# Kernel optimization log

Hardware: AMD Instinct MI355X
Metric: run time of the kernel (lower is better)

## Reference

```python
import jax, jax.numpy as jnp
import numpy as np

DIM = 768
HEADS = 12
HEAD_DIM = DIM // HEADS
B, S = 2, 2048
EPS = 1e-5


def _layernorm(x, w, b):
    mu = jnp.mean(x, axis=-1, keepdims=True)
    var = jnp.mean(jnp.square(x - mu), axis=-1, keepdims=True)
    return (x - mu) * jax.lax.rsqrt(var + EPS) * w + b


def setup_inputs() -> dict:
    key = jax.random.key(0)
    ks = jax.random.split(key, 16)
    sc = 1.0 / np.sqrt(DIM)
    inp = {
        'x': jax.random.normal(ks[0], (B, S, DIM), jnp.float32),
        'bias': jax.random.normal(ks[1], (HEADS, B, S, S), jnp.float32),
        'mask': jax.random.randint(ks[2], (1, B, S, S), 0, 2, jnp.int32),
        'ln1_w': jnp.ones((DIM,), jnp.float32),
        'ln1_b': jnp.zeros((DIM,), jnp.float32),
        'wq': jax.random.normal(ks[3], (DIM, DIM), jnp.float32) * sc,
        'bq': jnp.zeros((DIM,), jnp.float32),
        'wk': jax.random.normal(ks[4], (DIM, DIM), jnp.float32) * sc,
        'bk': jnp.zeros((DIM,), jnp.float32),
        'wv': jax.random.normal(ks[5], (DIM, DIM), jnp.float32) * sc,
        'bv': jnp.zeros((DIM,), jnp.float32),
        'wo': jax.random.normal(ks[6], (DIM, DIM), jnp.float32) * sc,
        'bo': jnp.zeros((DIM,), jnp.float32),
        'ln2_w': jnp.ones((DIM,), jnp.float32),
        'ln2_b': jnp.zeros((DIM,), jnp.float32),
        'w1': jax.random.normal(ks[7], (DIM, DIM), jnp.float32) * sc,
        'b1': jnp.zeros((DIM,), jnp.float32),
        'w2': jax.random.normal(ks[8], (DIM, DIM), jnp.float32) * sc,
        'b2': jnp.zeros((DIM,), jnp.float32),
    }
    return inp


def _split_heads(t):
    # [B,S,D] -> [H,B,S,Dh]  (matches torch view + permute(2,0,1,3))
    return t.reshape(B, S, HEADS, HEAD_DIM).transpose(2, 0, 1, 3)


def reference(x, bias, mask, ln1_w, ln1_b, wq, bq, wk, bk, wv, bv, wo, bo,
              ln2_w, ln2_b, w1, b1, w2, b2):
    xn = _layernorm(x, ln1_w, ln1_b)
    q = _split_heads(xn @ wq + bq)
    k = _split_heads(xn @ wk + bk)
    v = _split_heads(xn @ wv + bv)
    # scores: [H,B,Sq,Sk]; bias added BEFORE scaling, then masked, then scaled softmax
    scores = jnp.einsum('hbqd,hbkd->hbqk', q, k) + bias
    scores = jnp.where(mask == 0, jnp.float32(-1e20), scores)
    probs = jax.nn.softmax(scores / np.sqrt(HEAD_DIM), axis=-1)
    attn = jnp.einsum('hbqk,hbkd->hbqd', probs, v)
    attn = attn.transpose(1, 2, 0, 3).reshape(B, S, DIM)
    x = x + (attn @ wo + bo)
    xn = _layernorm(x, ln2_w, ln2_b)
    h = jax.nn.relu(xn @ w1 + b1)
    x = x + (h @ w2 + b2)
    return x
```

## Files before the change

### kernel.cpp

```cpp
#include <hip/hip_runtime.h>
#include <math.h>

#define DIMM 768
#define SEQ 2048
#define BATB 2
#define NHEAD 12
#define DHEAD 64
#define ROWS 4096

typedef __attribute__((ext_vector_type(8))) short bf16x8;
typedef __attribute__((ext_vector_type(4))) float f32x4;
typedef unsigned short ushort_t;
typedef unsigned int uint_t;

union U16 { int4 i; ushort_t u[8]; };

__device__ __forceinline__ ushort_t f2b(float f) {
    uint_t u = __float_as_uint(f);
    return (ushort_t)((u + 0x7FFFu + ((u >> 16) & 1u)) >> 16);
}

struct WPtrs { const float* s[6]; };

__global__ __launch_bounds__(256) void wtrans_k(WPtrs wp, ushort_t* __restrict__ dst)
{
    __shared__ float T[64][65];
    int wi = blockIdx.z;
    const float* in = wp.s[wi];
    ushort_t* out = dst + (size_t)wi * (DIMM * DIMM);
    int kb = blockIdx.y * 64, nb = blockIdx.x * 64;
    int t = threadIdx.x;
    int kl = t >> 4, nl = (t & 15) * 4;
    #pragma unroll
    for (int it = 0; it < 4; it++) {
        float4 a = *(const float4*)&in[(size_t)(kb + kl + it * 16) * DIMM + nb + nl];
        T[kl + it * 16][nl + 0] = a.x;
        T[kl + it * 16][nl + 1] = a.y;
        T[kl + it * 16][nl + 2] = a.z;
        T[kl + it * 16][nl + 3] = a.w;
    }
    __syncthreads();
    int no = t >> 2, ko = (t & 3) * 16;
    #pragma unroll
    for (int j = 0; j < 2; j++) {
        U16 u;
        #pragma unroll
        for (int c = 0; c < 8; c++) u.u[c] = f2b(T[ko + j * 8 + c][no]);
        *(int4*)&out[(size_t)(nb + no) * DIMM + kb + ko + j * 8] = u.i;
    }
}

__global__ __launch_bounds__(256) void ln_k(const float* __restrict__ x,
                                            const float* __restrict__ w,
                                            const float* __restrict__ b,
                                            ushort_t* __restrict__ out)
{
    int row = blockIdx.x;
    int tid = threadIdx.x;
    const float* xr = x + (size_t)row * DIMM;
    float v0 = xr[tid], v1 = xr[tid + 256], v2 = xr[tid + 512];
    float s  = v0 + v1 + v2;
    float ss = v0 * v0 + v1 * v1 + v2 * v2;
    #pragma unroll
    for (int off = 32; off > 0; off >>= 1) {
        s  += __shfl_down(s,  off);
        ss += __shfl_down(ss, off);
    }
    __shared__ float ws_[4], wss_[4];
    __shared__ float mu_s, rs_s;
    int lane = tid & 63, wid = tid >> 6;
    if (lane == 0) { ws_[wid] = s; wss_[wid] = ss; }
    __syncthreads();
    if (tid == 0) {
        float S1 = ws_[0] + ws_[1] + ws_[2] + ws_[3];
        float S2 = wss_[0] + wss_[1] + wss_[2] + wss_[3];
        float m = S1 * (1.0f / DIMM);
        float var = S2 * (1.0f / DIMM) - m * m;
        mu_s = m;
        rs_s = rsqrtf(var + 1e-5f);
    }
    __syncthreads();
    float mu = mu_s, rs = rs_s;
    ushort_t* orow = out + (size_t)row * DIMM;
    orow[tid]       = f2b((v0 - mu) * rs * w[tid]       + b[tid]);
    orow[tid + 256] = f2b((v1 - mu) * rs * w[tid + 256] + b[tid + 256]);
    orow[tid + 512] = f2b((v2 - mu) * rs * w[tid + 512] + b[tid + 512]);
}

template<int ASRC, int OMODE, bool RELU, bool RES>
__global__ __launch_bounds__(256) void mgemm_k(const ushort_t* __restrict__ A,
                                               const ushort_t* __restrict__ BT,
                                               const float* __restrict__ bias,
                                               const float* __restrict__ res,
                                               void* __restrict__ outv)
{
    __shared__ alignas(16) ushort_t Asl[8 * 64 * 8];
    __shared__ alignas(16) ushort_t Bsl[8 * 64 * 8];
    int tid = threadIdx.x;
    int lane = tid & 63, w = tid >> 6;
    int colBase = blockIdx.x * 64, rowBase = blockIdx.y * 64;

    f32x4 acc[4];
    #pragma unroll
    for (int nt = 0; nt < 4; nt++) { f32x4 z = {0.f, 0.f, 0.f, 0.f}; acc[nt] = z; }

    int sm = tid >> 2;
    int sko = (tid & 3) * 16;

    for (int kt = 0; kt < DIMM; kt += 64) {
        #pragma unroll
        for (int j = 0; j < 2; j++) {
            int k = sko + j * 8;
            size_t gidx;
            if (ASRC == 1) {
                gidx = (size_t)(rowBase + sm) * DIMM + kt + k;
            } else {
                int r = rowBase + sm, kg = kt + k;
                gidx = ((size_t)((kg >> 6) * BATB + (r >> 11)) * SEQ + (r & 2047)) * DHEAD + (kg & 63);
            }
            int4 a = *(const int4*)&A[gidx];
            int ln = (sm & 15) | (((k & 31) >> 3) << 4);
            int slot = ((sm >> 4) << 1) | (k >> 5);
            *(int4*)&Asl[(slot * 64 + ln) * 8] = a;
        }
        #pragma unroll
        for (int j = 0; j < 2; j++) {
            int k = sko + j * 8;
            int4 b = *(const int4*)&BT[(size_t)(colBase + sm) * DIMM + kt + k];
            int ln = (sm & 15) | (((k & 31) >> 3) << 4);
            int slot = (k >> 5) * 4 + (sm >> 4);
            *(int4*)&Bsl[(slot * 64 + ln) * 8] = b;
        }
        __syncthreads();
        bf16x8 a0 = *(bf16x8*)&Asl[((w * 2 + 0) * 64 + lane) * 8];
        bf16x8 a1 = *(bf16x8*)&Asl[((w * 2 + 1) * 64 + lane) * 8];
        #pragma unroll
        for (int nt = 0; nt < 4; nt++) {
            bf16x8 b0 = *(bf16x8*)&Bsl[((0 * 4 + nt) * 64 + lane) * 8];
            bf16x8 b1 = *(bf16x8*)&Bsl[((1 * 4 + nt) * 64 + lane) * 8];
            acc[nt] = __builtin_amdgcn_mfma_f32_16x16x32_bf16(a0, b0, acc[nt], 0, 0, 0);
            acc[nt] = __builtin_amdgcn_mfma_f32_16x16x32_bf16(a1, b1, acc[nt], 0, 0, 0);
        }
        __syncthreads();
    }
    int col_l = lane & 15, quad = lane >> 4;
    #pragma unroll
    for (int nt = 0; nt < 4; nt++) {
        int n = colBase + nt * 16 + col_l;
        float bn = bias[n];
        #pragma unroll
        for (int r = 0; r < 4; r++) {
            int row = rowBase + w * 16 + quad * 4 + r;
            float v = acc[nt][r] + bn;
            if (RELU) v = fmaxf(v, 0.0f);
            if (RES)  v += res[(size_t)row * DIMM + n];
            if (OMODE == 0) {
                ((float*)outv)[(size_t)row * DIMM + n] = v;
            } else if (OMODE == 1) {
                ((ushort_t*)outv)[(size_t)row * DIMM + n] = f2b(v);
            } else {
                ((ushort_t*)outv)[((size_t)((n >> 6) * BATB + (row >> 11)) * SEQ + (row & 2047)) * DHEAD + (n & 63)] = f2b(v);
            }
        }
    }
}

__global__ __launch_bounds__(256) void attn_k(const ushort_t* __restrict__ q,
                                              const ushort_t* __restrict__ k,
                                              const ushort_t* __restrict__ v,
                                              const float* __restrict__ bias,
                                              const int* __restrict__ mask,
                                              ushort_t* __restrict__ out)
{
    __shared__ alignas(16) ushort_t Kf[8 * 64 * 8];
    __shared__ alignas(16) ushort_t Vf[8 * 64 * 8];
    __shared__ alignas(16) ushort_t Pf[8 * 64 * 8];
    int tid = threadIdx.x, lane = tid & 63, w = tid >> 6;
    int col_l = lane & 15, quad = lane >> 4;
    int qbase = blockIdx.x * 64;
    int hb = blockIdx.y;
    const ushort_t* qp = q + (size_t)hb * SEQ * DHEAD;
    const ushort_t* kp = k + (size_t)hb * SEQ * DHEAD;
    const ushort_t* vp = v + (size_t)hb * SEQ * DHEAD;
    const float* bp = bias + (size_t)hb * SEQ * SEQ;
    const int*   mp = mask + (size_t)(hb & 1) * SEQ * SEQ;

    bf16x8 qF0 = *(const bf16x8*)&qp[(size_t)(qbase + w * 16 + col_l) * DHEAD + (quad * 8)];
    bf16x8 qF1 = *(const bf16x8*)&qp[(size_t)(qbase + w * 16 + col_l) * DHEAD + 32 + (quad * 8)];

    f32x4 O[4];
    #pragma unroll
    for (int nt = 0; nt < 4; nt++) { f32x4 z = {0.f, 0.f, 0.f, 0.f}; O[nt] = z; }
    float m_run[4], l_run[4];
    #pragma unroll
    for (int r = 0; r < 4; r++) { m_run[r] = -1e30f; l_run[r] = 0.0f; }

    int sn = tid >> 2, sko = (tid & 3) * 16;
    int j0 = (tid >> 3) * 2, e0 = (tid & 7) * 8;

    for (int kvb = 0; kvb < SEQ; kvb += 64) {
        #pragma unroll
        for (int jj = 0; jj < 2; jj++) {
            int kk = sko + jj * 8;
            int4 kd = *(const int4*)&kp[(size_t)(kvb + sn) * DHEAD + kk];
            int slot = (kk >> 5) * 4 + (sn >> 4);
            int ln = (sn & 15) | (((kk & 31) >> 3) << 4);
            *(int4*)&Kf[(slot * 64 + ln) * 8] = kd;
        }
        {
            U16 g0, g1;
            g0.i = *(const int4*)&vp[(size_t)(kvb + j0) * DHEAD + e0];
            g1.i = *(const int4*)&vp[(size_t)(kvb + j0 + 1) * DHEAD + e0];
            int js = j0 >> 5, grp = (j0 & 31) >> 3, i0 = j0 & 7;
            #pragma unroll
            for (int c = 0; c < 8; c++) {
                int n = e0 + c;
                uint_t pk = (uint_t)g0.u[c] | ((uint_t)g1.u[c] << 16);
                int idx = ((js * 4 + (n >> 4)) * 64 + ((n & 15) | (grp << 4))) * 8 + i0;
                *(uint_t*)&Vf[idx] = pk;
            }
        }
        float bl[4][4]; int ml[4][4];
        #pragma unroll
        for (int nt = 0; nt < 4; nt++) {
            int col = kvb + nt * 16 + col_l;
            #pragma unroll
            for (int r = 0; r < 4; r++) {
                int qrow = qbase + w * 16 + quad * 4 + r;
                bl[nt][r] = bp[(size_t)qrow * SEQ + col];
                ml[nt][r] = mp[(size_t)qrow * SEQ + col];
            }
        }
        __syncthreads();
        f32x4 S[4];
        #pragma unroll
        for (int nt = 0; nt < 4; nt++) {
            bf16x8 b0 = *(bf16x8*)&Kf[((0 * 4 + nt) * 64 + lane) * 8];
            bf16x8 b1 = *(bf16x8*)&Kf[((1 * 4 + nt) * 64 + lane) * 8];
            f32x4 z = {0.f, 0.f, 0.f, 0.f};
            z = __builtin_amdgcn_mfma_f32_16x16x32_bf16(qF0, b0, z, 0, 0, 0);
            S[nt] = __builtin_amdgcn_mfma_f32_16x16x32_bf16(qF1, b1, z, 0, 0, 0);
        }
        float lg[4][4];
        #pragma unroll
        for (int nt = 0; nt < 4; nt++)
            #pragma unroll
            for (int r = 0; r < 4; r++)
                lg[nt][r] = ml[nt][r] ? (S[nt][r] + bl[nt][r]) * 0.125f : -1.25e19f;
        float alpha[4];
        #pragma unroll
        for (int r = 0; r < 4; r++) {
            float mx = fmaxf(fmaxf(lg[0][r], lg[1][r]), fmaxf(lg[2][r], lg[3][r]));
            mx = fmaxf(mx, __shfl_xor(mx, 1));
            mx = fmaxf(mx, __shfl_xor(mx, 2));
            mx = fmaxf(mx, __shfl_xor(mx, 4));
            mx = fmaxf(mx, __shfl_xor(mx, 8));
            float mnew = fmaxf(m_run[r], mx);
            alpha[r] = __expf(m_run[r] - mnew);
            m_run[r] = mnew;
            float rs = 0.0f;
            #pragma unroll
            for (int nt = 0; nt < 4; nt++) {
                float p = __expf(lg[nt][r] - mnew);
                lg[nt][r] = p;
                rs += p;
            }
            rs += __shfl_xor(rs, 1);
            rs += __shfl_xor(rs, 2);
            rs += __shfl_xor(rs, 4);
            rs += __shfl_xor(rs, 8);
            l_run[r] = l_run[r] * alpha[r] + rs;
        }
        #pragma unroll
        for (int nt = 0; nt < 4; nt++)
            #pragma unroll
            for (int r = 0; r < 4; r++)
                O[nt][r] *= alpha[r];
        #pragma unroll
        for (int nt = 0; nt < 4; nt++) {
            int j = nt * 16 + col_l;
            #pragma unroll
            for (int r = 0; r < 4; r++) {
                ushort_t pu = f2b(lg[nt][r]);
                uint_t po = (uint_t)(unsigned)__shfl_xor((int)pu, 1);
                if ((lane & 1) == 0) {
                    int m = quad * 4 + r;
                    int idx = ((w * 2 + (j >> 5)) * 64 + (m | (((j & 31) >> 3) << 4))) * 8 + (j & 7);
                    *(uint_t*)&Pf[idx] = (uint_t)pu | (po << 16);
                }
            }
        }
        #pragma unroll
        for (int js = 0; js < 2; js++) {
            bf16x8 pF = *(bf16x8*)&Pf[((w * 2 + js) * 64 + lane) * 8];
            #pragma unroll
            for (int nt = 0; nt < 4; nt++) {
                bf16x8 vF = *(bf16x8*)&Vf[((js * 4 + nt) * 64 + lane) * 8];
                O[nt] = __builtin_amdgcn_mfma_f32_16x16x32_bf16(pF, vF, O[nt], 0, 0, 0);
            }
        }
        __syncthreads();
    }
    float inv[4];
    #pragma unroll
    for (int r = 0; r < 4; r++) inv[r] = 1.0f / l_run[r];
    #pragma unroll
    for (int nt = 0; nt < 4; nt++)
        #pragma unroll
        for (int r = 0; r < 4; r++) {
            int row = qbase + w * 16 + quad * 4 + r;
            out[((size_t)hb * SEQ + row) * DHEAD + nt * 16 + col_l] = f2b(O[nt][r] * inv[r]);
        }
}

extern "C" void kernel_launch(void* const* d_in, const int* in_sizes, int n_in,
                              void* d_out, int out_size, void* d_ws, size_t ws_size,
                              hipStream_t stream)
{
    const float* x    = (const float*)d_in[0];
    const float* bias = (const float*)d_in[1];
    const int*   mask = (const int*)d_in[2];
    const float* ln1w = (const float*)d_in[3];
    const float* ln1b = (const float*)d_in[4];
    const float* wq   = (const float*)d_in[5];
    const float* bq   = (const float*)d_in[6];
    const float* wk   = (const float*)d_in[7];
    const float* bk   = (const float*)d_in[8];
    const float* wv   = (const float*)d_in[9];
    const float* bv   = (const float*)d_in[10];
    const float* wo   = (const float*)d_in[11];
    const float* bo   = (const float*)d_in[12];
    const float* ln2w = (const float*)d_in[13];
    const float* ln2b = (const float*)d_in[14];
    const float* w1   = (const float*)d_in[15];
    const float* b1   = (const float*)d_in[16];
    const float* w2   = (const float*)d_in[17];
    const float* b2   = (const float*)d_in[18];

    const size_t WSZ = (size_t)DIMM * DIMM;
    const size_t ABUF = (size_t)ROWS * DIMM;

    ushort_t* wsu  = (ushort_t*)d_ws;
    ushort_t* wT   = wsu;
    ushort_t* qb   = wsu + 6 * WSZ;
    ushort_t* kbuf = qb + ABUF;
    ushort_t* vbuf = kbuf + ABUF;
    ushort_t* xn1  = vbuf + ABUF;
    float*    x1   = (float*)(xn1 + ABUF);
    ushort_t* hid  = qb;

    WPtrs wp; wp.s[0] = wq; wp.s[1] = wk; wp.s[2] = wv; wp.s[3] = wo; wp.s[4] = w1; wp.s[5] = w2;

    dim3 gg(12, 64), gb(256);
    wtrans_k<<<dim3(12, 12, 6), 256, 0, stream>>>(wp, wT);
    ln_k<<<ROWS, 256, 0, stream>>>(x, ln1w, ln1b, xn1);
    mgemm_k<1, 2, false, false><<<gg, gb, 0, stream>>>(xn1, wT + 0 * WSZ, bq, nullptr, qb);
    mgemm_k<1, 2, false, false><<<gg, gb, 0, stream>>>(xn1, wT + 1 * WSZ, bk, nullptr, kbuf);
    mgemm_k<1, 2, false, false><<<gg, gb, 0, stream>>>(xn1, wT + 2 * WSZ, bv, nullptr, vbuf);
    attn_k<<<dim3(32, 24), 256, 0, stream>>>(qb, kbuf, vbuf, bias, mask, xn1);
    mgemm_k<2, 0, false, true><<<gg, gb, 0, stream>>>(xn1, wT + 3 * WSZ, bo, x, x1);
    ln_k<<<ROWS, 256, 0, stream>>>(x1, ln2w, ln2b, xn1);
    mgemm_k<1, 1, true, false><<<gg, gb, 0, stream>>>(xn1, wT + 4 * WSZ, b1, nullptr, hid);
    mgemm_k<1, 0, false, true><<<gg, gb, 0, stream>>>(hid, wT + 5 * WSZ, b2, x1, (float*)d_out);
}
```

Before: 750.6 us.

## Load GEMM fragments directly from global memory and fuse QKV projections

The GEMM kernel drops its shared-memory staging and barriers. Each wave now loads its MFMA A/B fragments straight from global memory, prefetching one K step ahead in registers. The three Q/K/V projections are merged into one launch over the concatenated transposed weights, with per-block bias selection. This removes LDS traffic, syncs and two launches, but now relies on caches for B reuse across waves and keeps only a shallow prefetch to hide global latency.

After: 896.7 us. +19.5%, slower.

```diff
diff --git a/kernel.cpp b/kernel.cpp
--- a/kernel.cpp
+++ b/kernel.cpp
@@ -21,6 +21,7 @@
 }
 
 struct WPtrs { const float* s[6]; };
+struct BPtrs { const float* p[3]; };
 
 __global__ __launch_bounds__(256) void wtrans_k(WPtrs wp, ushort_t* __restrict__ dst)
 {
@@ -87,67 +88,71 @@
     orow[tid + 512] = f2b((v2 - mu) * rs * w[tid + 512] + b[tid + 512]);
 }
 
-template<int ASRC, int OMODE, bool RELU, bool RES>
+template<int ASRC, int OMODE, bool RELU, bool RES, int NB>
 __global__ __launch_bounds__(256) void mgemm_k(const ushort_t* __restrict__ A,
                                                const ushort_t* __restrict__ BT,
-                                               const float* __restrict__ bias,
+                                               BPtrs bias,
                                                const float* __restrict__ res,
                                                void* __restrict__ outv)
 {
-    __shared__ alignas(16) ushort_t Asl[8 * 64 * 8];
-    __shared__ alignas(16) ushort_t Bsl[8 * 64 * 8];
     int tid = threadIdx.x;
     int lane = tid & 63, w = tid >> 6;
-    int colBase = blockIdx.x * 64, rowBase = blockIdx.y * 64;
+    int col_l = lane & 15, quad = lane >> 4;
+    int q8 = quad * 8;
+    int colBase = blockIdx.x * 64;
+    int rowBase = blockIdx.y * 64;
+    int arow = rowBase + w * 16 + col_l;
+
+    size_t abase;
+    if (ASRC == 1) abase = (size_t)arow * DIMM;
+    else           abase = ((size_t)(arow >> 11) * SEQ + (arow & 2047)) * DHEAD;
+    const size_t HSTR = (size_t)BATB * SEQ * DHEAD;
+
+    size_t bbase[4];
+    #pragma unroll
+    for (int nt = 0; nt < 4; nt++)
+        bbase[nt] = (size_t)(colBase + nt * 16 + col_l) * DIMM;
 
     f32x4 acc[4];
     #pragma unroll
     for (int nt = 0; nt < 4; nt++) { f32x4 z = {0.f, 0.f, 0.f, 0.f}; acc[nt] = z; }
 
-    int sm = tid >> 2;
-    int sko = (tid & 3) * 16;
-
-    for (int kt = 0; kt < DIMM; kt += 64) {
-        #pragma unroll
-        for (int j = 0; j < 2; j++) {
-            int k = sko + j * 8;
-            size_t gidx;
-            if (ASRC == 1) {
-                gidx = (size_t)(rowBase + sm) * DIMM + kt + k;
-            } else {
-                int r = rowBase + sm, kg = kt + k;
-                gidx = ((size_t)((kg >> 6) * BATB + (r >> 11)) * SEQ + (r & 2047)) * DHEAD + (kg & 63);
-            }
-            int4 a = *(const int4*)&A[gidx];
-            int ln = (sm & 15) | (((k & 31) >> 3) << 4);
-            int slot = ((sm >> 4) << 1) | (k >> 5);
-            *(int4*)&Asl[(slot * 64 + ln) * 8] = a;
-        }
-        #pragma unroll
-        for (int j = 0; j < 2; j++) {
-            int k = sko + j * 8;
-            int4 b = *(const int4*)&BT[(size_t)(colBase + sm) * DIMM + kt + k];
-            int ln = (sm & 15) | (((k & 31) >> 3) << 4);
-            int slot = (k >> 5) * 4 + (sm >> 4);
-            *(int4*)&Bsl[(slot * 64 + ln) * 8] = b;
-        }
-        __syncthreads();
-        bf16x8 a0 = *(bf16x8*)&Asl[((w * 2 + 0) * 64 + lane) * 8];
-        bf16x8 a1 = *(bf16x8*)&Asl[((w * 2 + 1) * 64 + lane) * 8];
-        #pragma unroll
-        for (int nt = 0; nt < 4; nt++) {
-            bf16x8 b0 = *(bf16x8*)&Bsl[((0 * 4 + nt) * 64 + lane) * 8];
-            bf16x8 b1 = *(bf16x8*)&Bsl[((1 * 4 + nt) * 64 + lane) * 8];
-            acc[nt] = __builtin_amdgcn_mfma_f32_16x16x32_bf16(a0, b0, acc[nt], 0, 0, 0);
-            acc[nt] = __builtin_amdgcn_mfma_f32_16x16x32_bf16(a1, b1, acc[nt], 0, 0, 0);
-        }
-        __syncthreads();
-    }
-    int col_l = lane & 15, quad = lane >> 4;
+    auto lda = [&](int kt) -> bf16x8 {
+        size_t off;
+        if (ASRC == 1) off = abase + kt + q8;
+        else           off = abase + (size_t)(kt >> 6) * HSTR + (kt & 63) + q8;
+        return *(const bf16x8*)&A[off];
+    };
+
+    bf16x8 aC = lda(0);
+    bf16x8 bC[4];
+    #pragma unroll
+    for (int nt = 0; nt < 4; nt++) bC[nt] = *(const bf16x8*)&BT[bbase[nt] + q8];
+
+    #pragma unroll
+    for (int kt = 0; kt < DIMM - 32; kt += 32) {
+        bf16x8 aN = lda(kt + 32);
+        bf16x8 bN[4];
+        #pragma unroll
+        for (int nt = 0; nt < 4; nt++) bN[nt] = *(const bf16x8*)&BT[bbase[nt] + kt + 32 + q8];
+        #pragma unroll
+        for (int nt = 0; nt < 4; nt++)
+            acc[nt] = __builtin_amdgcn_mfma_f32_16x16x32_bf16(aC, bC[nt], acc[nt], 0, 0, 0);
+        aC = aN;
+        #pragma unroll
+        for (int nt = 0; nt < 4; nt++) bC[nt] = bN[nt];
+    }
+    #pragma unroll
+    for (int nt = 0; nt < 4; nt++)
+        acc[nt] = __builtin_amdgcn_mfma_f32_16x16x32_bf16(aC, bC[nt], acc[nt], 0, 0, 0);
+
+    int wi = (NB == 3) ? (int)(blockIdx.x / 12) : 0;
+    const float* bp_ = bias.p[wi];
+    int nLoc0 = colBase - wi * DIMM;
     #pragma unroll
     for (int nt = 0; nt < 4; nt++) {
         int n = colBase + nt * 16 + col_l;
-        float bn = bias[n];
+        float bn = bp_[nLoc0 + nt * 16 + col_l];
         #pragma unroll
         for (int r = 0; r < 4; r++) {
             int row = rowBase + w * 16 + quad * 4 + r;
@@ -350,16 +355,18 @@
     ushort_t* hid  = qb;
 
     WPtrs wp; wp.s[0] = wq; wp.s[1] = wk; wp.s[2] = wv; wp.s[3] = wo; wp.s[4] = w1; wp.s[5] = w2;
+    BPtrs bqkv; bqkv.p[0] = bq; bqkv.p[1] = bk; bqkv.p[2] = bv;
+    BPtrs bbo;  bbo.p[0]  = bo; bbo.p[1]  = bo; bbo.p[2]  = bo;
+    BPtrs bb1;  bb1.p[0]  = b1; bb1.p[1]  = b1; bb1.p[2]  = b1;
+    BPtrs bb2;  bb2.p[0]  = b2; bb2.p[1]  = b2; bb2.p[2]  = b2;
 
     dim3 gg(12, 64), gb(256);
     wtrans_k<<<dim3(12, 12, 6), 256, 0, stream>>>(wp, wT);
     ln_k<<<ROWS, 256, 0, stream>>>(x, ln1w, ln1b, xn1);
-    mgemm_k<1, 2, false, false><<<gg, gb, 0, stream>>>(xn1, wT + 0 * WSZ, bq, nullptr, qb);
-    mgemm_k<1, 2, false, false><<<gg, gb, 0, stream>>>(xn1, wT + 1 * WSZ, bk, nullptr, kbuf);
-    mgemm_k<1, 2, false, false><<<gg, gb, 0, stream>>>(xn1, wT + 2 * WSZ, bv, nullptr, vbuf);
+    mgemm_k<1, 2, false, false, 3><<<dim3(36, 64), gb, 0, stream>>>(xn1, wT, bqkv, nullptr, qb);
     attn_k<<<dim3(32, 24), 256, 0, stream>>>(qb, kbuf, vbuf, bias, mask, xn1);
-    mgemm_k<2, 0, false, true><<<gg, gb, 0, stream>>>(xn1, wT + 3 * WSZ, bo, x, x1);
+    mgemm_k<2, 0, false, true, 1><<<gg, gb, 0, stream>>>(xn1, wT + 3 * WSZ, bbo, x, x1);
     ln_k<<<ROWS, 256, 0, stream>>>(x1, ln2w, ln2b, xn1);
-    mgemm_k<1, 1, true, false><<<gg, gb, 0, stream>>>(xn1, wT + 4 * WSZ, b1, nullptr, hid);
-    mgemm_k<1, 0, false, true><<<gg, gb, 0, stream>>>(hid, wT + 5 * WSZ, b2, x1, (float*)d_out);
-}
+    mgemm_k<1, 1, true, false, 1><<<gg, gb, 0, stream>>>(xn1, wT + 4 * WSZ, bb1, nullptr, hid);
+    mgemm_k<1, 0, false, true, 1><<<gg, gb, 0, stream>>>(hid, wT + 5 * WSZ, bb2, x1, (float*)d_out);
+}
```
